# Kernel optimization log

Hardware: AMD Instinct MI355X
Metric: run time of the kernel (lower is better)

Reference implementation:

```python
import jax, jax.numpy as jnp
import numpy as np

HIDDEN = 1024
D_INNER = 2048
DT_RANK = 64
STATE = 16
KCONV = 4


def setup_inputs() -> dict:
    key = jax.random.key(0)
    ks = jax.random.split(key, 9)
    s = lambda k, shape, sc=0.02: jax.random.normal(k, shape, dtype=jnp.float32) * sc
    return {
        "x": jax.random.normal(ks[0], (2, 1024, HIDDEN), dtype=jnp.float32),
        "in_proj_w": s(ks[1], (2 * D_INNER, HIDDEN)),
        "conv_w": s(ks[2], (D_INNER, 1, KCONV), 0.2),
        "conv_b": s(ks[3], (D_INNER,), 0.1),
        "x_proj_w": s(ks[4], (DT_RANK + 2 * STATE, D_INNER)),
        "dt_proj_w": s(ks[5], (D_INNER, DT_RANK), 0.1),
        "dt_proj_b": s(ks[6], (D_INNER,), 0.1),
        "A_log": s(ks[7], (D_INNER, STATE), 0.5),
        "out_proj_w": s(ks[8], (HIDDEN, D_INNER)),
    }


def _selective_scan(u, delta, A, B, C):
    # u, delta: (b,l,d); A: (d,n); B, C: (b,l,n)
    deltaA = jnp.exp(delta[..., None] * A)               # (b,l,d,n)
    dBu = (delta * u)[..., None] * B[:, :, None, :]      # (b,l,d,n)
    # scan over time axis; carry h: (b,d,n)
    deltaA_t = jnp.moveaxis(deltaA, 1, 0)                # (l,b,d,n)
    dBu_t = jnp.moveaxis(dBu, 1, 0)                      # (l,b,d,n)
    C_t = jnp.moveaxis(C, 1, 0)                          # (l,b,n)

    def step(h, inp):
        dA_i, dBu_i, C_i = inp
        h = dA_i * h + dBu_i
        y = jnp.einsum('bdn,bn->bd', h, C_i)
        return h, y

    h0 = jnp.zeros(u.shape[:1] + u.shape[2:] + (A.shape[1],), dtype=u.dtype)
    _, ys = jax.lax.scan(step, h0, (deltaA_t, dBu_t, C_t))
    return jnp.moveaxis(ys, 0, 1)                        # (b,l,d)


def reference(x, in_proj_w, conv_w, conv_b, x_proj_w, dt_proj_w, dt_proj_b, A_log, out_proj_w):
    b, l, _ = x.shape
    xr = x @ in_proj_w.T                                 # (b,l,2*d_inner)
    xs, res = jnp.split(xr, 2, axis=-1)
    # causal depthwise conv1d: pad left k-1 (matches padding=k-1 then [:l])
    xc = jnp.moveaxis(xs, 1, 2)                          # (b,d,l)
    xc = jax.lax.conv_general_dilated(
        xc, conv_w, window_strides=(1,), padding=[(KCONV - 1, 0)],
        feature_group_count=D_INNER,
        dimension_numbers=('NCH', 'OIH', 'NCH'))
    xc = xc + conv_b[None, :, None]
    xs = jnp.moveaxis(xc, 2, 1)                          # (b,l,d)
    xs = jax.nn.silu(xs)
    x_dbl = xs @ x_proj_w.T                              # (b,l,dt_rank+2n)
    dt, B, C = jnp.split(x_dbl, [DT_RANK, DT_RANK + STATE], axis=-1)
    delta = jax.nn.softplus(dt @ dt_proj_w.T + dt_proj_b)
    A = -jnp.exp(A_log.astype(jnp.float32))
    y = _selective_scan(xs, delta, A, B, C)
    y = y * jax.nn.silu(res)
    return y @ out_proj_w.T
```

## Files before the change

### kernel.cpp

```cpp
#include <hip/hip_runtime.h>

typedef unsigned short u16;
typedef __bf16 bf16x8 __attribute__((ext_vector_type(8)));
typedef float f32x4 __attribute__((ext_vector_type(4)));

__device__ inline float bf2f(u16 u) {
    unsigned int x = ((unsigned int)u) << 16;
    return __builtin_bit_cast(float, x);
}
__device__ inline u16 f2bf(float f) {
    unsigned int x = __builtin_bit_cast(unsigned int, f);
    return (u16)((x + 0x7FFFu + ((x >> 16) & 1u)) >> 16);
}
__device__ inline float sigm(float v) { return 1.f / (1.f + __expf(-v)); }

__device__ __forceinline__ void gload16(const void* g, void* l) {
    __builtin_amdgcn_global_load_lds(
        (const __attribute__((address_space(1))) void*)g,
        (__attribute__((address_space(3))) void*)l, 16, 0, 0);
}

__device__ inline uint4 pack8(const float* p) {
    const float4* q = (const float4*)p;
    float4 a = q[0], b = q[1];
    union { u16 h[8]; uint4 v; } u;
    u.h[0] = f2bf(a.x); u.h[1] = f2bf(a.y); u.h[2] = f2bf(a.z); u.h[3] = f2bf(a.w);
    u.h[4] = f2bf(b.x); u.h[5] = f2bf(b.y); u.h[6] = f2bf(b.z); u.h[7] = f2bf(b.w);
    return u.v;
}

__global__ __launch_bounds__(256)
void cvt_bf16(const float* __restrict__ in, u16* __restrict__ out)
{
    int i = blockIdx.x * 256 + threadIdx.x;
    ((uint4*)out)[i] = pack8(in + (size_t)i * 8);
}
__global__ __launch_bounds__(256)
void cvt_pad_xproj(const float* __restrict__ in, u16* __restrict__ out)
{
    int i = blockIdx.x * 256 + threadIdx.x;
    int row = (i * 8) >> 11;
    ((uint4*)out)[i] = (row < 96) ? pack8(in + (size_t)row * 2048 + ((i * 8) & 2047))
                                  : make_uint4(0u, 0u, 0u, 0u);
}

template<int EPI, bool OUTF32>
__global__ __launch_bounds__(256, 2)
void gemm2(const u16* __restrict__ A, int lda,
           const u16* __restrict__ B, int ldb,
           void* __restrict__ Cout, int ldc,
           int N, int ksplit, size_t zElems,
           const float* __restrict__ bias)
{
    __shared__ u16 sA[128][64];
    __shared__ u16 sB[128][64];

    const int tid  = threadIdx.x;
    const int lane = tid & 63;
    const int wave = tid >> 6;
    const int wm = (wave >> 1) * 64;
    const int wn = (wave & 1) * 64;
    const int m0 = blockIdx.y * 128;
    const int n0 = blockIdx.x * 128;
    const int lm = lane & 15;
    const int g  = lane >> 4;
    const int k0 = blockIdx.z * ksplit;

    const int rr = lane >> 3;
    const int sl = lane & 7;
    const int xsl = sl ^ rr;
    const u16* gA = A + (size_t)(m0 + wave * 8 + rr) * lda + k0 + xsl * 8;
    const u16* gB = B + (size_t)(n0 + wave * 8 + rr) * ldb + k0 + xsl * 8;
    const int ldsRow = (wave * 8) * 128;

    f32x4 acc[4][4] = {};

    for (int kb = 0; kb < ksplit; kb += 64) {
        #pragma unroll
        for (int c = 0; c < 4; ++c) {
            gload16(gA + (size_t)c * 32 * lda + kb, (char*)sA + c * 4096 + ldsRow);
            gload16(gB + (size_t)c * 32 * ldb + kb, (char*)sB + c * 4096 + ldsRow);
        }
        __syncthreads();

        bf16x8 af[2][4], bfr[2][4];
        #pragma unroll
        for (int h = 0; h < 2; ++h) {
            #pragma unroll
            for (int i = 0; i < 4; ++i) {
                int ra = wm + i * 16 + lm;
                int rb = wn + i * 16 + lm;
                int chunk = (((h << 2) | g) ^ (lm & 7)) << 4;
                af[h][i]  = *(const bf16x8*)((const char*)sA + ra * 128 + chunk);
                bfr[h][i] = *(const bf16x8*)((const char*)sB + rb * 128 + chunk);
            }
        }
        #pragma unroll
        for (int h = 0; h < 2; ++h)
            #pragma unroll
            for (int i = 0; i < 4; ++i)
                #pragma unroll
                for (int j = 0; j < 4; ++j)
                    acc[i][j] = __builtin_amdgcn_mfma_f32_16x16x32_bf16(af[h][i], bfr[h][j], acc[i][j], 0, 0, 0);
        __syncthreads();
    }

    #pragma unroll
    for (int i = 0; i < 4; ++i) {
        int crow = m0 + wm + i * 16 + ((lane >> 4) << 2);
        #pragma unroll
        for (int j = 0; j < 4; ++j) {
            int ccol = n0 + wn + j * 16 + lm;
            if (ccol < N) {
                #pragma unroll
                for (int r = 0; r < 4; ++r) {
                    float v = acc[i][j][r];
                    if (EPI == 2 && ccol >= 2048) v *= sigm(v);
                    size_t off = (size_t)blockIdx.z * zElems + (size_t)(crow + r) * ldc + ccol;
                    if (OUTF32) ((float*)Cout)[off] = v;
                    else        ((u16*)Cout)[off]   = f2bf(v);
                }
            }
        }
    }
}

__global__ __launch_bounds__(256)
void dt_delta(const u16* __restrict__ xdbl, const float* __restrict__ dtw,
              const float* __restrict__ bias, u16* __restrict__ out)
{
    const int tid = threadIdx.x;
    const int d   = blockIdx.x * 256 + tid;
    const int t0  = blockIdx.y * 16;

    __shared__ float s_x[16][64];

    if (tid < 128) {
        int tok = tid >> 3, ch = tid & 7;
        uint4 v = *(const uint4*)&xdbl[(size_t)(t0 + tok) * 96 + ch * 8];
        const u16* h = (const u16*)&v;
        #pragma unroll
        for (int e = 0; e < 8; ++e) s_x[tok][ch * 8 + e] = bf2f(h[e]);
    }

    float w[64];
    {
        const float4* wp = (const float4*)(dtw + (size_t)d * 64);
        #pragma unroll
        for (int q = 0; q < 16; ++q) {
            float4 v = wp[q];
            w[q * 4 + 0] = v.x; w[q * 4 + 1] = v.y;
            w[q * 4 + 2] = v.z; w[q * 4 + 3] = v.w;
        }
    }
    const float bd = bias[d];
    __syncthreads();

    for (int tok = 0; tok < 16; ++tok) {
        float a0 = bd, a1 = 0.f, a2 = 0.f, a3 = 0.f;
        const float4* xv4 = (const float4*)s_x[tok];
        #pragma unroll
        for (int q = 0; q < 16; ++q) {
            float4 xv = xv4[q];
            a0 = fmaf(w[q * 4 + 0], xv.x, a0);
            a1 = fmaf(w[q * 4 + 1], xv.y, a1);
            a2 = fmaf(w[q * 4 + 2], xv.z, a2);
            a3 = fmaf(w[q * 4 + 3], xv.w, a3);
        }
        float v = (a0 + a1) + (a2 + a3);
        v = (v > 20.f) ? v : log1pf(__expf(v));
        out[(size_t)(t0 + tok) * 4096 + d] = f2bf(v);
    }
}

__global__ __launch_bounds__(256)
void reduce96(const float* __restrict__ splits, u16* __restrict__ xdbl)
{
    int i = blockIdx.x * 256 + threadIdx.x;
    float acc = 0.f;
    #pragma unroll
    for (int z = 0; z < 8; ++z) acc += splits[(size_t)z * 196608 + i];
    xdbl[i] = f2bf(acc);
}

__global__ __launch_bounds__(256)
void reduce_out(const u16* __restrict__ parts, float* __restrict__ out)
{
    int i = blockIdx.x * 256 + threadIdx.x;
    float acc[8] = {};
    #pragma unroll
    for (int z = 0; z < 4; ++z) {
        uint4 v = ((const uint4*)(parts + (size_t)z * 2097152))[i];
        const u16* h = (const u16*)&v;
        #pragma unroll
        for (int e = 0; e < 8; ++e) acc[e] += bf2f(h[e]);
    }
    float4* o = (float4*)(out + (size_t)i * 8);
    o[0] = make_float4(acc[0], acc[1], acc[2], acc[3]);
    o[1] = make_float4(acc[4], acc[5], acc[6], acc[7]);
}

__global__ __launch_bounds__(256)
void conv_silu(const u16* __restrict__ xr, const float* __restrict__ w,
               const float* __restrict__ bias, u16* __restrict__ xs)
{
    int idx = blockIdx.x * 256 + threadIdx.x;
    int d = idx & 2047, t = (idx >> 11) & 1023, b = idx >> 21;
    const u16* base = xr + (size_t)b * 1024 * 4096;
    float acc = bias[d];
    #pragma unroll
    for (int j = 0; j < 4; ++j) {
        int ti = t - 3 + j;
        if (ti >= 0) acc = fmaf(w[d * 4 + j], bf2f(base[(size_t)ti * 4096 + d]), acc);
    }
    xs[idx] = f2bf(acc * sigm(acc));
}

template<int PHC>
__global__ __launch_bounds__(256)
void scan_chunk(const u16* __restrict__ deltag, u16* __restrict__ xsg,
                const u16* __restrict__ xdbl, const float* __restrict__ A_log,
                const u16* __restrict__ xr, float* __restrict__ summ,
                float* __restrict__ ssum)
{
    const int tid = threadIdx.x;
    const int d0 = blockIdx.x * 256;
    const int c  = blockIdx.y;
    const int b  = blockIdx.z;
    const int d  = d0 + tid;
    const int tok0 = b * 1024 + c * 32;

    __shared__ u16 s_del[32][256];
    __shared__ u16 s_uu[32][256];
    __shared__ u16 s_bc[32][32];
    __shared__ u16 s_res[PHC ? 32 : 1][PHC ? 256 : 1];
    __shared__ u16 s_y[PHC ? 32 : 1][PHC ? 256 : 1];

    for (int i = tid; i < 1024; i += 256) {
        int tl = i >> 5, v = i & 31;
        size_t tok = (size_t)(tok0 + tl);
        *(uint4*)&s_del[tl][v * 8] = *(const uint4*)&deltag[tok * 4096 + d0 + v * 8];
        *(uint4*)&s_uu[tl][v * 8]  = *(const uint4*)&xsg[tok * 2048 + d0 + v * 8];
        if (PHC)
            *(uint4*)&s_res[tl][v * 8] = *(const uint4*)&xr[tok * 4096 + 2048 + d0 + v * 8];
    }
    for (int i = tid; i < 1024; i += 256) {
        int tl = i >> 5, j = i & 31;
        s_bc[tl][j] = xdbl[(size_t)(tok0 + tl) * 96 + 64 + j];
    }

    float Ar[16], h[16];
    {
        const float4* Ap = (const float4*)(A_log + (size_t)d * 16);
        #pragma unroll
        for (int q = 0; q < 4; ++q) {
            float4 a = Ap[q];
            Ar[q * 4 + 0] = -__expf(a.x); Ar[q * 4 + 1] = -__expf(a.y);
            Ar[q * 4 + 2] = -__expf(a.z); Ar[q * 4 + 3] = -__expf(a.w);
        }
    }
    if (PHC) {
        const float4* hp = (const float4*)&summ[((size_t)(b * 32 + c) * 2048 + d) * 16];
        #pragma unroll
        for (int q = 0; q < 4; ++q) {
            float4 v = hp[q];
            h[q * 4 + 0] = v.x; h[q * 4 + 1] = v.y; h[q * 4 + 2] = v.z; h[q * 4 + 3] = v.w;
        }
    } else {
        #pragma unroll
        for (int n = 0; n < 16; ++n) h[n] = 0.f;
    }
    __syncthreads();

    float S = 0.f;
    #pragma unroll 4
    for (int tl = 0; tl < 32; ++tl) {
        float dlt = bf2f(s_del[tl][tid]);
        float du = dlt * bf2f(s_uu[tl][tid]);
        if (!PHC) S += dlt;
        #pragma unroll
        for (int n = 0; n < 16; ++n)
            h[n] = fmaf(__expf(dlt * Ar[n]), h[n], du * bf2f(s_bc[tl][n]));
        if (PHC) {
            float y = 0.f;
            #pragma unroll
            for (int n = 0; n < 16; ++n)
                y = fmaf(h[n], bf2f(s_bc[tl][16 + n]), y);
            s_y[tl][tid] = f2bf(y * bf2f(s_res[tl][tid]));
        }
    }

    if (!PHC) {
        float4* bp = (float4*)&summ[((size_t)(b * 32 + c) * 2048 + d) * 16];
        #pragma unroll
        for (int q = 0; q < 4; ++q)
            bp[q] = make_float4(h[q * 4], h[q * 4 + 1], h[q * 4 + 2], h[q * 4 + 3]);
        ssum[(size_t)(b * 32 + c) * 2048 + d] = S;
    } else {
        __syncthreads();
        for (int i = tid; i < 1024; i += 256) {
            int tl = i >> 5, v = i & 31;
            *(uint4*)&xsg[(size_t)(tok0 + tl) * 2048 + d0 + v * 8] = *(uint4*)&s_y[tl][v * 8];
        }
    }
}

__global__ __launch_bounds__(256)
void scan_phaseB(float* __restrict__ summ, const float* __restrict__ ssum,
                 const float* __restrict__ A_log)
{
    int g = blockIdx.x * 256 + threadIdx.x;
    int n = g & 15;
    int d = (g >> 4) & 2047;
    int b = g >> 15;
    float An = -__expf(A_log[(size_t)d * 16 + n]);
    float h = 0.f;
    for (int c = 0; c < 32; ++c) {
        size_t idx = ((size_t)(b * 32 + c) * 2048 + d) * 16 + n;
        float bc = summ[idx];
        float Sc = ssum[(size_t)(b * 32 + c) * 2048 + d];
        summ[idx] = h;
        h = fmaf(__expf(An * Sc), h, bc);
    }
}

__global__ void sentinel_kernel(float* out, float v) { out[0] = v; }

extern "C" void kernel_launch(void* const* d_in, const int* in_sizes, int n_in,
                              void* d_out, int out_size, void* d_ws, size_t ws_size,
                              hipStream_t stream)
{
    const float* x         = (const float*)d_in[0];
    const float* in_w      = (const float*)d_in[1];
    const float* conv_w    = (const float*)d_in[2];
    const float* conv_b    = (const float*)d_in[3];
    const float* xproj_w   = (const float*)d_in[4];
    const float* dtproj_w  = (const float*)d_in[5];
    const float* dtproj_b  = (const float*)d_in[6];
    const float* A_log     = (const float*)d_in[7];
    const float* outproj_w = (const float*)d_in[8];
    float* out = (float*)d_out;

    static const int EXP[9] = {2097152, 4194304, 8192, 2048, 196608, 131072, 2048, 32768, 2097152};
    int bad = -1;
    if (n_in != 9) bad = 9;
    else { for (int i = 0; i < 9; ++i) if (in_sizes[i] != EXP[i]) { bad = i; break; } }
    if (bad < 0 && out_size != 2097152) bad = 10;
    if (bad < 0 && ws_size < 34734080u) bad = 11;
    if (bad >= 0) {
        sentinel_kernel<<<1, 1, 0, stream>>>(out, 131072.f * (1.f + (float)bad / 16.f));
        return;
    }

    char* ws = (char*)d_ws;
    u16*   xr      = (u16*)(ws);
    u16*   xs      = (u16*)(ws + 16777216);
    u16*   xdbl    = (u16*)(ws + 25165824);
    char*  R       = ws + 25559040;
    u16*   x_bf    = xs;
    u16*   inw_bf  = (u16*)(R);
    u16*   xpw_bf  = (u16*)(R + 8388608);
    float* splits  = (float*)(R);
    float* summ    = (float*)(R);
    float* ssum    = (float*)(R + 8388608);
    u16*   opw_bf  = (u16*)(R);
    u16*   oparts  = xr;

    cvt_bf16<<<1024, 256, 0, stream>>>(x, x_bf);
    cvt_bf16<<<2048, 256, 0, stream>>>(in_w, inw_bf);
    cvt_pad_xproj<<<128, 256, 0, stream>>>(xproj_w, xpw_bf);
    gemm2<2, false><<<dim3(32, 16, 1), 256, 0, stream>>>(
        x_bf, 1024, inw_bf, 1024, xr, 4096, 4096, 1024, 0, nullptr);
    conv_silu<<<16384, 256, 0, stream>>>(xr, conv_w, conv_b, xs);
    gemm2<0, true><<<dim3(1, 16, 8), 256, 0, stream>>>(
        xs, 2048, xpw_bf, 2048, splits, 96, 96, 256, 196608, nullptr);
    reduce96<<<768, 256, 0, stream>>>(splits, xdbl);
    dt_delta<<<dim3(8, 128), 256, 0, stream>>>(xdbl, dtproj_w, dtproj_b, xr);
    scan_chunk<0><<<dim3(8, 32, 2), 256, 0, stream>>>(xr, xs, xdbl, A_log, xr, summ, ssum);
    scan_phaseB<<<256, 256, 0, stream>>>(summ, ssum, A_log);
    scan_chunk<1><<<dim3(8, 32, 2), 256, 0, stream>>>(xr, xs, xdbl, A_log, xr, summ, ssum);
    cvt_bf16<<<1024, 256, 0, stream>>>(outproj_w, opw_bf);
    gemm2<0, false><<<dim3(8, 16, 4), 256, 0, stream>>>(
        xs, 2048, opw_bf, 2048, oparts, 1024, 1024, 512, 2097152, nullptr);
    reduce_out<<<1024, 256, 0, stream>>>(oparts, out);
}
```

Measured before the change: 260.6 us.

## Fuse scan phases cooperatively, merge conversions, vectorize conv, swizzle GEMM tiles

Merges the three input conversion kernels plus a conv-weight transpose into one launch. conv_silu is vectorized to process 8 channels per thread using transposed weights. GEMM blocks are remapped with a grid swizzle for better cache locality. The three scan kernels are fused into one cooperative kernel with grid-wide syncs, with a multi-launch fallback. This trades launch overhead for grid-sync cost and higher LDS use per scan block.

```diff
diff --git a/kernel.cpp b/kernel.cpp
--- a/kernel.cpp
+++ b/kernel.cpp
@@ -1,4 +1,7 @@
 #include <hip/hip_runtime.h>
+#include <hip/hip_cooperative_groups.h>
+
+namespace cg = cooperative_groups;
 
 typedef unsigned short u16;
 typedef __bf16 bf16x8 __attribute__((ext_vector_type(8)));
@@ -30,18 +33,34 @@
 }
 
 __global__ __launch_bounds__(256)
+void cvt_front(const float* __restrict__ x, const float* __restrict__ inw,
+               const float* __restrict__ xpw, const float* __restrict__ convw,
+               u16* __restrict__ x_bf, u16* __restrict__ inw_bf,
+               u16* __restrict__ xpw_bf, float* __restrict__ wt)
+{
+    int bk = blockIdx.x, tid = threadIdx.x;
+    if (bk < 1024) {
+        int i = bk * 256 + tid;
+        ((uint4*)x_bf)[i] = pack8(x + (size_t)i * 8);
+    } else if (bk < 3072) {
+        int i = (bk - 1024) * 256 + tid;
+        ((uint4*)inw_bf)[i] = pack8(inw + (size_t)i * 8);
+    } else if (bk < 3200) {
+        int i = (bk - 3072) * 256 + tid;
+        int row = (i * 8) >> 11;
+        ((uint4*)xpw_bf)[i] = (row < 96) ? pack8(xpw + (size_t)row * 2048 + ((i * 8) & 2047))
+                                         : make_uint4(0u, 0u, 0u, 0u);
+    } else {
+        int i = (bk - 3200) * 256 + tid;
+        wt[(i & 3) * 2048 + (i >> 2)] = convw[i];
+    }
+}
+
+__global__ __launch_bounds__(256)
 void cvt_bf16(const float* __restrict__ in, u16* __restrict__ out)
 {
     int i = blockIdx.x * 256 + threadIdx.x;
     ((uint4*)out)[i] = pack8(in + (size_t)i * 8);
-}
-__global__ __launch_bounds__(256)
-void cvt_pad_xproj(const float* __restrict__ in, u16* __restrict__ out)
-{
-    int i = blockIdx.x * 256 + threadIdx.x;
-    int row = (i * 8) >> 11;
-    ((uint4*)out)[i] = (row < 96) ? pack8(in + (size_t)row * 2048 + ((i * 8) & 2047))
-                                  : make_uint4(0u, 0u, 0u, 0u);
 }
 
 template<int EPI, bool OUTF32>
@@ -58,10 +77,21 @@
     const int tid  = threadIdx.x;
     const int lane = tid & 63;
     const int wave = tid >> 6;
+
+    int nxy = gridDim.x * gridDim.y;
+    int id  = blockIdx.y * gridDim.x + blockIdx.x;
+    int bx, by;
+    if ((nxy & 7) == 0) {
+        int cpx = nxy >> 3;
+        int swz = (id & 7) * cpx + (id >> 3);
+        bx = swz % gridDim.x;
+        by = swz / gridDim.x;
+    } else { bx = blockIdx.x; by = blockIdx.y; }
+
     const int wm = (wave >> 1) * 64;
     const int wn = (wave & 1) * 64;
-    const int m0 = blockIdx.y * 128;
-    const int n0 = blockIdx.x * 128;
+    const int m0 = by * 128;
+    const int n0 = bx * 128;
     const int lm = lane & 15;
     const int g  = lane >> 4;
     const int k0 = blockIdx.z * ksplit;
@@ -201,56 +231,75 @@
 }
 
 __global__ __launch_bounds__(256)
-void conv_silu(const u16* __restrict__ xr, const float* __restrict__ w,
+void conv_silu(const u16* __restrict__ xr, const float* __restrict__ wt,
                const float* __restrict__ bias, u16* __restrict__ xs)
 {
-    int idx = blockIdx.x * 256 + threadIdx.x;
-    int d = idx & 2047, t = (idx >> 11) & 1023, b = idx >> 21;
-    const u16* base = xr + (size_t)b * 1024 * 4096;
-    float acc = bias[d];
+    int gi = blockIdx.x * 256 + threadIdx.x;
+    int d  = (gi & 255) * 8;
+    int t  = (gi >> 8) & 1023;
+    int b  = gi >> 18;
+    const u16* base = xr + (size_t)b * 4194304 + d;
+    float acc[8];
+    {
+        const float4* bp = (const float4*)(bias + d);
+        float4 b0 = bp[0], b1 = bp[1];
+        acc[0]=b0.x; acc[1]=b0.y; acc[2]=b0.z; acc[3]=b0.w;
+        acc[4]=b1.x; acc[5]=b1.y; acc[6]=b1.z; acc[7]=b1.w;
+    }
     #pragma unroll
     for (int j = 0; j < 4; ++j) {
         int ti = t - 3 + j;
-        if (ti >= 0) acc = fmaf(w[d * 4 + j], bf2f(base[(size_t)ti * 4096 + d]), acc);
-    }
-    xs[idx] = f2bf(acc * sigm(acc));
-}
-
-template<int PHC>
-__global__ __launch_bounds__(256)
-void scan_chunk(const u16* __restrict__ deltag, u16* __restrict__ xsg,
+        if (ti >= 0) {
+            uint4 v = *(const uint4*)(base + (size_t)ti * 4096);
+            const u16* h = (const u16*)&v;
+            const float4* wp = (const float4*)(wt + j * 2048 + d);
+            float4 w0 = wp[0], w1 = wp[1];
+            float w8[8] = {w0.x, w0.y, w0.z, w0.w, w1.x, w1.y, w1.z, w1.w};
+            #pragma unroll
+            for (int e = 0; e < 8; ++e) acc[e] = fmaf(w8[e], bf2f(h[e]), acc[e]);
+        }
+    }
+    union { u16 h[8]; uint4 v; } o;
+    #pragma unroll
+    for (int e = 0; e < 8; ++e) { float v = acc[e]; o.h[e] = f2bf(v * sigm(v)); }
+    ((uint4*)xs)[gi] = o.v;
+}
+
+template<int MODE>
+__global__ __launch_bounds__(256, 2)
+void scan_fused(const u16* __restrict__ deltag, u16* __restrict__ xsg,
                 const u16* __restrict__ xdbl, const float* __restrict__ A_log,
                 const u16* __restrict__ xr, float* __restrict__ summ,
                 float* __restrict__ ssum)
 {
     const int tid = threadIdx.x;
+    __shared__ u16 s_del[32][256];
+    __shared__ u16 s_uu[32][256];
+    __shared__ u16 s_bc[32][32];
+    __shared__ u16 s_res[32][256];
+    __shared__ u16 s_y[32][256];
+
     const int d0 = blockIdx.x * 256;
     const int c  = blockIdx.y;
     const int b  = blockIdx.z;
     const int d  = d0 + tid;
     const int tok0 = b * 1024 + c * 32;
 
-    __shared__ u16 s_del[32][256];
-    __shared__ u16 s_uu[32][256];
-    __shared__ u16 s_bc[32][32];
-    __shared__ u16 s_res[PHC ? 32 : 1][PHC ? 256 : 1];
-    __shared__ u16 s_y[PHC ? 32 : 1][PHC ? 256 : 1];
-
-    for (int i = tid; i < 1024; i += 256) {
-        int tl = i >> 5, v = i & 31;
-        size_t tok = (size_t)(tok0 + tl);
-        *(uint4*)&s_del[tl][v * 8] = *(const uint4*)&deltag[tok * 4096 + d0 + v * 8];
-        *(uint4*)&s_uu[tl][v * 8]  = *(const uint4*)&xsg[tok * 2048 + d0 + v * 8];
-        if (PHC)
-            *(uint4*)&s_res[tl][v * 8] = *(const uint4*)&xr[tok * 4096 + 2048 + d0 + v * 8];
-    }
-    for (int i = tid; i < 1024; i += 256) {
-        int tl = i >> 5, j = i & 31;
-        s_bc[tl][j] = xdbl[(size_t)(tok0 + tl) * 96 + 64 + j];
-    }
-
-    float Ar[16], h[16];
-    {
+    float Ar[16];
+
+    if (MODE != 1) {
+        for (int i = tid; i < 1024; i += 256) {
+            int tl = i >> 5, v = i & 31;
+            size_t tok = (size_t)(tok0 + tl);
+            *(uint4*)&s_del[tl][v * 8] = *(const uint4*)&deltag[tok * 4096 + d0 + v * 8];
+            *(uint4*)&s_uu[tl][v * 8]  = *(const uint4*)&xsg[tok * 2048 + d0 + v * 8];
+            if (MODE != 0)
+                *(uint4*)&s_res[tl][v * 8] = *(const uint4*)&xr[tok * 4096 + 2048 + d0 + v * 8];
+        }
+        for (int i = tid; i < 1024; i += 256) {
+            int tl = i >> 5, j = i & 31;
+            s_bc[tl][j] = xdbl[(size_t)(tok0 + tl) * 96 + 64 + j];
+        }
         const float4* Ap = (const float4*)(A_log + (size_t)d * 16);
         #pragma unroll
         for (int q = 0; q < 4; ++q) {
@@ -258,69 +307,79 @@
             Ar[q * 4 + 0] = -__expf(a.x); Ar[q * 4 + 1] = -__expf(a.y);
             Ar[q * 4 + 2] = -__expf(a.z); Ar[q * 4 + 3] = -__expf(a.w);
         }
-    }
-    if (PHC) {
-        const float4* hp = (const float4*)&summ[((size_t)(b * 32 + c) * 2048 + d) * 16];
-        #pragma unroll
-        for (int q = 0; q < 4; ++q) {
-            float4 v = hp[q];
-            h[q * 4 + 0] = v.x; h[q * 4 + 1] = v.y; h[q * 4 + 2] = v.z; h[q * 4 + 3] = v.w;
-        }
-    } else {
+        __syncthreads();
+    }
+
+    if (MODE == 0 || MODE == 3) {
+        float h[16];
         #pragma unroll
         for (int n = 0; n < 16; ++n) h[n] = 0.f;
-    }
-    __syncthreads();
-
-    float S = 0.f;
-    #pragma unroll 4
-    for (int tl = 0; tl < 32; ++tl) {
-        float dlt = bf2f(s_del[tl][tid]);
-        float du = dlt * bf2f(s_uu[tl][tid]);
-        if (!PHC) S += dlt;
-        #pragma unroll
-        for (int n = 0; n < 16; ++n)
-            h[n] = fmaf(__expf(dlt * Ar[n]), h[n], du * bf2f(s_bc[tl][n]));
-        if (PHC) {
-            float y = 0.f;
+        float S = 0.f;
+        #pragma unroll 4
+        for (int tl = 0; tl < 32; ++tl) {
+            float dlt = bf2f(s_del[tl][tid]);
+            float du = dlt * bf2f(s_uu[tl][tid]);
+            S += dlt;
             #pragma unroll
             for (int n = 0; n < 16; ++n)
-                y = fmaf(h[n], bf2f(s_bc[tl][16 + n]), y);
-            s_y[tl][tid] = f2bf(y * bf2f(s_res[tl][tid]));
-        }
-    }
-
-    if (!PHC) {
+                h[n] = fmaf(__expf(dlt * Ar[n]), h[n], du * bf2f(s_bc[tl][n]));
+        }
         float4* bp = (float4*)&summ[((size_t)(b * 32 + c) * 2048 + d) * 16];
         #pragma unroll
         for (int q = 0; q < 4; ++q)
             bp[q] = make_float4(h[q * 4], h[q * 4 + 1], h[q * 4 + 2], h[q * 4 + 3]);
         ssum[(size_t)(b * 32 + c) * 2048 + d] = S;
-    } else {
+    }
+
+    if (MODE == 3) { __threadfence(); cg::this_grid().sync(); }
+
+    if (MODE == 1 || MODE == 3) {
+        int bid = (blockIdx.z * gridDim.y + blockIdx.y) * gridDim.x + blockIdx.x;
+        int gid = bid * 256 + tid;
+        if (gid < 65536) {
+            int n  = gid & 15;
+            int dd = (gid >> 4) & 2047;
+            int bb = gid >> 15;
+            float An = -__expf(A_log[(size_t)dd * 16 + n]);
+            float hh = 0.f;
+            for (int cc = 0; cc < 32; ++cc) {
+                size_t idx = ((size_t)(bb * 32 + cc) * 2048 + dd) * 16 + n;
+                float bc = summ[idx];
+                float Sc = ssum[(size_t)(bb * 32 + cc) * 2048 + dd];
+                summ[idx] = hh;
+                hh = fmaf(__expf(An * Sc), hh, bc);
+            }
+        }
+    }
+
+    if (MODE == 3) { __threadfence(); cg::this_grid().sync(); }
+
+    if (MODE == 2 || MODE == 3) {
+        float h[16];
+        const float4* hp = (const float4*)&summ[((size_t)(b * 32 + c) * 2048 + d) * 16];
+        #pragma unroll
+        for (int q = 0; q < 4; ++q) {
+            float4 v = hp[q];
+            h[q * 4 + 0] = v.x; h[q * 4 + 1] = v.y;
+            h[q * 4 + 2] = v.z; h[q * 4 + 3] = v.w;
+        }
+        #pragma unroll 4
+        for (int tl = 0; tl < 32; ++tl) {
+            float dlt = bf2f(s_del[tl][tid]);
+            float du = dlt * bf2f(s_uu[tl][tid]);
+            float y = 0.f;
+            #pragma unroll
+            for (int n = 0; n < 16; ++n) {
+                h[n] = fmaf(__expf(dlt * Ar[n]), h[n], du * bf2f(s_bc[tl][n]));
+                y = fmaf(h[n], bf2f(s_bc[tl][16 + n]), y);
+            }
+            s_y[tl][tid] = f2bf(y * bf2f(s_res[tl][tid]));
+        }
         __syncthreads();
         for (int i = tid; i < 1024; i += 256) {
             int tl = i >> 5, v = i & 31;
             *(uint4*)&xsg[(size_t)(tok0 + tl) * 2048 + d0 + v * 8] = *(uint4*)&s_y[tl][v * 8];
         }
-    }
-}
-
-__global__ __launch_bounds__(256)
-void scan_phaseB(float* __restrict__ summ, const float* __restrict__ ssum,
-                 const float* __restrict__ A_log)
-{
-    int g = blockIdx.x * 256 + threadIdx.x;
-    int n = g & 15;
-    int d = (g >> 4) & 2047;
-    int b = g >> 15;
-    float An = -__expf(A_log[(size_t)d * 16 + n]);
-    float h = 0.f;
-    for (int c = 0; c < 32; ++c) {
-        size_t idx = ((size_t)(b * 32 + c) * 2048 + d) * 16 + n;
-        float bc = summ[idx];
-        float Sc = ssum[(size_t)(b * 32 + c) * 2048 + d];
-        summ[idx] = h;
-        h = fmaf(__expf(An * Sc), h, bc);
     }
 }
 
@@ -360,25 +419,33 @@
     u16*   x_bf    = xs;
     u16*   inw_bf  = (u16*)(R);
     u16*   xpw_bf  = (u16*)(R + 8388608);
+    float* wt      = (float*)(R + 8912896);
     float* splits  = (float*)(R);
     float* summ    = (float*)(R);
     float* ssum    = (float*)(R + 8388608);
     u16*   opw_bf  = (u16*)(R);
     u16*   oparts  = xr;
 
-    cvt_bf16<<<1024, 256, 0, stream>>>(x, x_bf);
-    cvt_bf16<<<2048, 256, 0, stream>>>(in_w, inw_bf);
-    cvt_pad_xproj<<<128, 256, 0, stream>>>(xproj_w, xpw_bf);
+    cvt_front<<<3232, 256, 0, stream>>>(x, in_w, xproj_w, conv_w,
+                                        x_bf, inw_bf, xpw_bf, wt);
     gemm2<2, false><<<dim3(32, 16, 1), 256, 0, stream>>>(
         x_bf, 1024, inw_bf, 1024, xr, 4096, 4096, 1024, 0, nullptr);
-    conv_silu<<<16384, 256, 0, stream>>>(xr, conv_w, conv_b, xs);
+    conv_silu<<<2048, 256, 0, stream>>>(xr, wt, conv_b, xs);
     gemm2<0, true><<<dim3(1, 16, 8), 256, 0, stream>>>(
         xs, 2048, xpw_bf, 2048, splits, 96, 96, 256, 196608, nullptr);
     reduce96<<<768, 256, 0, stream>>>(splits, xdbl);
     dt_delta<<<dim3(8, 128), 256, 0, stream>>>(xdbl, dtproj_w, dtproj_b, xr);
-    scan_chunk<0><<<dim3(8, 32, 2), 256, 0, stream>>>(xr, xs, xdbl, A_log, xr, summ, ssum);
-    scan_phaseB<<<256, 256, 0, stream>>>(summ, ssum, A_log);
-    scan_chunk<1><<<dim3(8, 32, 2), 256, 0, stream>>>(xr, xs, xdbl, A_log, xr, summ, ssum);
+    {
+        void* sargs[] = { (void*)&xr, (void*)&xs, (void*)&xdbl, (void*)&A_log,
+                          (void*)&xr, (void*)&summ, (void*)&ssum };
+        hipError_t ce = hipLaunchCooperativeKernel(scan_fused<3>,
+                            dim3(8, 32, 2), dim3(256, 1, 1), sargs, 0u, stream);
+        if (ce != hipSuccess) {
+            scan_fused<0><<<dim3(8, 32, 2), 256, 0, stream>>>(xr, xs, xdbl, A_log, xr, summ, ssum);
+            scan_fused<1><<<dim3(256, 1, 1), 256, 0, stream>>>(xr, xs, xdbl, A_log, xr, summ, ssum);
+            scan_fused<2><<<dim3(8, 32, 2), 256, 0, stream>>>(xr, xs, xdbl, A_log, xr, summ, ssum);
+        }
+    }
     cvt_bf16<<<1024, 256, 0, stream>>>(outproj_w, opw_bf);
     gemm2<0, false><<<dim3(8, 16, 4), 256, 0, stream>>>(
         xs, 2048, opw_bf, 2048, oparts, 1024, 1024, 512, 2097152, nullptr);
```

Result: slower. 491.0 us (+88.4%).

## Fuse front conversions, vectorize conv_silu, and swizzle GEMM block order

Applied to the files above, without the earlier changes.

Merges the three fp32-to-bf16 conversion launches and a conv-weight transpose into one kernel, which cuts launch overhead. conv_silu now has each thread handle 8 channels using 16-byte loads and the transposed weights, replacing scalar gathers. The GEMM remaps block indices in groups of 8 so that concurrently running blocks touch nearby tiles, aiming for better L2 reuse. The wt buffer lives in the workspace region after xpw_bf, which must not overlap other buffers that are live at the same time.

```diff
diff --git a/kernel.cpp b/kernel.cpp
--- a/kernel.cpp
+++ b/kernel.cpp
@@ -30,18 +30,34 @@
 }
 
 __global__ __launch_bounds__(256)
+void cvt_front(const float* __restrict__ x, const float* __restrict__ inw,
+               const float* __restrict__ xpw, const float* __restrict__ convw,
+               u16* __restrict__ x_bf, u16* __restrict__ inw_bf,
+               u16* __restrict__ xpw_bf, float* __restrict__ wt)
+{
+    int bk = blockIdx.x, tid = threadIdx.x;
+    if (bk < 1024) {
+        int i = bk * 256 + tid;
+        ((uint4*)x_bf)[i] = pack8(x + (size_t)i * 8);
+    } else if (bk < 3072) {
+        int i = (bk - 1024) * 256 + tid;
+        ((uint4*)inw_bf)[i] = pack8(inw + (size_t)i * 8);
+    } else if (bk < 3200) {
+        int i = (bk - 3072) * 256 + tid;
+        int row = (i * 8) >> 11;
+        ((uint4*)xpw_bf)[i] = (row < 96) ? pack8(xpw + (size_t)row * 2048 + ((i * 8) & 2047))
+                                         : make_uint4(0u, 0u, 0u, 0u);
+    } else {
+        int i = (bk - 3200) * 256 + tid;
+        wt[(i & 3) * 2048 + (i >> 2)] = convw[i];
+    }
+}
+
+__global__ __launch_bounds__(256)
 void cvt_bf16(const float* __restrict__ in, u16* __restrict__ out)
 {
     int i = blockIdx.x * 256 + threadIdx.x;
     ((uint4*)out)[i] = pack8(in + (size_t)i * 8);
-}
-__global__ __launch_bounds__(256)
-void cvt_pad_xproj(const float* __restrict__ in, u16* __restrict__ out)
-{
-    int i = blockIdx.x * 256 + threadIdx.x;
-    int row = (i * 8) >> 11;
-    ((uint4*)out)[i] = (row < 96) ? pack8(in + (size_t)row * 2048 + ((i * 8) & 2047))
-                                  : make_uint4(0u, 0u, 0u, 0u);
 }
 
 template<int EPI, bool OUTF32>
@@ -58,10 +74,21 @@
     const int tid  = threadIdx.x;
     const int lane = tid & 63;
     const int wave = tid >> 6;
+
+    int nxy = gridDim.x * gridDim.y;
+    int id  = blockIdx.y * gridDim.x + blockIdx.x;
+    int bx, by;
+    if ((nxy & 7) == 0) {
+        int cpx = nxy >> 3;
+        int swz = (id & 7) * cpx + (id >> 3);
+        bx = swz % gridDim.x;
+        by = swz / gridDim.x;
+    } else { bx = blockIdx.x; by = blockIdx.y; }
+
     const int wm = (wave >> 1) * 64;
     const int wn = (wave & 1) * 64;
-    const int m0 = blockIdx.y * 128;
-    const int n0 = blockIdx.x * 128;
+    const int m0 = by * 128;
+    const int n0 = bx * 128;
     const int lm = lane & 15;
     const int g  = lane >> 4;
     const int k0 = blockIdx.z * ksplit;
@@ -201,19 +228,38 @@
 }
 
 __global__ __launch_bounds__(256)
-void conv_silu(const u16* __restrict__ xr, const float* __restrict__ w,
+void conv_silu(const u16* __restrict__ xr, const float* __restrict__ wt,
                const float* __restrict__ bias, u16* __restrict__ xs)
 {
-    int idx = blockIdx.x * 256 + threadIdx.x;
-    int d = idx & 2047, t = (idx >> 11) & 1023, b = idx >> 21;
-    const u16* base = xr + (size_t)b * 1024 * 4096;
-    float acc = bias[d];
+    int gi = blockIdx.x * 256 + threadIdx.x;
+    int d  = (gi & 255) * 8;
+    int t  = (gi >> 8) & 1023;
+    int b  = gi >> 18;
+    const u16* base = xr + (size_t)b * 4194304 + d;
+    float acc[8];
+    {
+        const float4* bp = (const float4*)(bias + d);
+        float4 b0 = bp[0], b1 = bp[1];
+        acc[0]=b0.x; acc[1]=b0.y; acc[2]=b0.z; acc[3]=b0.w;
+        acc[4]=b1.x; acc[5]=b1.y; acc[6]=b1.z; acc[7]=b1.w;
+    }
     #pragma unroll
     for (int j = 0; j < 4; ++j) {
         int ti = t - 3 + j;
-        if (ti >= 0) acc = fmaf(w[d * 4 + j], bf2f(base[(size_t)ti * 4096 + d]), acc);
-    }
-    xs[idx] = f2bf(acc * sigm(acc));
+        if (ti >= 0) {
+            uint4 v = *(const uint4*)(base + (size_t)ti * 4096);
+            const u16* h = (const u16*)&v;
+            const float4* wp = (const float4*)(wt + j * 2048 + d);
+            float4 w0 = wp[0], w1 = wp[1];
+            float w8[8] = {w0.x, w0.y, w0.z, w0.w, w1.x, w1.y, w1.z, w1.w};
+            #pragma unroll
+            for (int e = 0; e < 8; ++e) acc[e] = fmaf(w8[e], bf2f(h[e]), acc[e]);
+        }
+    }
+    union { u16 h[8]; uint4 v; } o;
+    #pragma unroll
+    for (int e = 0; e < 8; ++e) { float v = acc[e]; o.h[e] = f2bf(v * sigm(v)); }
+    ((uint4*)xs)[gi] = o.v;
 }
 
 template<int PHC>
@@ -360,18 +406,18 @@
     u16*   x_bf    = xs;
     u16*   inw_bf  = (u16*)(R);
     u16*   xpw_bf  = (u16*)(R + 8388608);
+    float* wt      = (float*)(R + 8912896);
     float* splits  = (float*)(R);
     float* summ    = (float*)(R);
     float* ssum    = (float*)(R + 8388608);
     u16*   opw_bf  = (u16*)(R);
     u16*   oparts  = xr;
 
-    cvt_bf16<<<1024, 256, 0, stream>>>(x, x_bf);
-    cvt_bf16<<<2048, 256, 0, stream>>>(in_w, inw_bf);
-    cvt_pad_xproj<<<128, 256, 0, stream>>>(xproj_w, xpw_bf);
+    cvt_front<<<3232, 256, 0, stream>>>(x, in_w, xproj_w, conv_w,
+                                        x_bf, inw_bf, xpw_bf, wt);
     gemm2<2, false><<<dim3(32, 16, 1), 256, 0, stream>>>(
         x_bf, 1024, inw_bf, 1024, xr, 4096, 4096, 1024, 0, nullptr);
-    conv_silu<<<16384, 256, 0, stream>>>(xr, conv_w, conv_b, xs);
+    conv_silu<<<2048, 256, 0, stream>>>(xr, wt, conv_b, xs);
     gemm2<0, true><<<dim3(1, 16, 8), 256, 0, stream>>>(
         xs, 2048, xpw_bf, 2048, splits, 96, 96, 256, 196608, nullptr);
     reduce96<<<768, 256, 0, stream>>>(splits, xdbl);
```

New measurement: 244.6 us. 6.2% less time.
